# Kernel tuning notes

Measured on AMD Instinct MI355X. Metric: run time of the kernel, lower is better.

Reference implementation:

```python
import jax, jax.numpy as jnp
import numpy as np

# Problem constants (match init_kwargs)
A = 64          # particles
H = 1024        # hidden width
B = 512         # batch of configurations
V0 = -5.0
SIGMA0 = 0.5
GAUSS_CONST = V0 / (np.sqrt(2.0 * np.pi) * SIGMA0)
INV_2SIG2 = 1.0 / (2.0 * SIGMA0 * SIGMA0)


def setup_inputs() -> dict:
    key = jax.random.key(0)
    ks = jax.random.split(key, 7)
    x = jax.random.normal(ks[0], (B, A), dtype=jnp.float32)
    # 3-layer tanh MLP params: log|psi| = MLP(x) -> scalar
    W1 = jax.random.normal(ks[1], (A, H), dtype=jnp.float32) / np.sqrt(A)
    b1 = jnp.zeros((H,), dtype=jnp.float32)
    W2 = jax.random.normal(ks[2], (H, H), dtype=jnp.float32) / np.sqrt(H)
    b2 = jnp.zeros((H,), dtype=jnp.float32)
    W3 = jax.random.normal(ks[3], (H, 1), dtype=jnp.float32) / np.sqrt(H)
    b3 = jnp.zeros((1,), dtype=jnp.float32)
    return {"x": x, "W1": W1, "b1": b1, "W2": W2, "b2": b2, "W3": W3, "b3": b3}


def _logabs(W1, b1, W2, b2, W3, b3, xs):
    # xs: [A] -> scalar log|psi|
    h = jnp.tanh(xs @ W1 + b1)
    h = jnp.tanh(h @ W2 + b2)
    return (h @ W3 + b3)[0]


def reference(x, W1, b1, W2, b2, W3, b3):
    def logabs(xs):
        return _logabs(W1, b1, W2, b2, W3, b3, xs)

    grad_fn = jax.grad(logabs)  # reverse-mode, like jacrev

    def per_sample(xs):
        g = grad_fn(xs)                       # [A]   dlogabs/dx
        hess = jax.jacrev(grad_fn)(xs)        # [A,A] nested jacrev (backward-over-backward)
        lap = jnp.trace(hess) + jnp.sum(g * g)
        kin = -0.5 * lap
        pot = 0.5 * jnp.sum(xs * xs)
        d = xs[None, :] - xs[:, None]          # [A,A] pairwise differences
        gint = GAUSS_CONST * jnp.sum(jnp.triu(jnp.exp(-(d * d) * INV_2SIG2), k=1))
        return kin + pot + gint

    return jax.vmap(per_sample)(x)  # [B] local energies
```

## Files before the change

kernel.cpp:

```cpp
#include <hip/hip_runtime.h>
#include <hip/hip_bf16.h>
#include <stdint.h>

#define AN 64
#define HN 1024
#define BN 512
#define GAUSS_CONST (-3.989422804014327f)
#define INV_2SIG2 2.0f

#define SA 192.0f
#define SB 768.0f
#define INVQ (1.0f / (SA * SB))

typedef __attribute__((ext_vector_type(8))) short short8;
typedef __attribute__((ext_vector_type(4))) short short4v;
typedef __attribute__((ext_vector_type(4))) float floatx4;
typedef __attribute__((ext_vector_type(4))) int intx4;

__device__ inline unsigned short f2bf(float f) {
  __hip_bfloat16 h = __float2bfloat16(f);
  return *reinterpret_cast<unsigned short*>(&h);
}

__device__ inline unsigned q8(float x, float s) {
  float xc = fminf(fmaxf(x * s, -127.f), 127.f);
  int qi = (int)rintf(xc);
  return (unsigned)(qi & 255);
}

__device__ inline void gload_lds16(const void* g, void* l) {
  __builtin_amdgcn_global_load_lds(
      (const __attribute__((address_space(1))) void*)g,
      (__attribute__((address_space(3))) void*)l, 16, 0, 0);
}

#define PH_BAR  asm volatile("s_barrier" ::: "memory")
#define WAITV2  asm volatile("s_waitcnt vmcnt(2)" ::: "memory")
#define WAITV0  asm volatile("s_waitcnt vmcnt(0)" ::: "memory")

__global__ __launch_bounds__(256) void k1(
    const float* __restrict__ x, const float* __restrict__ W1,
    const float* __restrict__ b1, const float* __restrict__ W2,
    unsigned short* __restrict__ h1bf, float* __restrict__ t1f,
    float* __restrict__ a1, float* __restrict__ potgint,
    unsigned char* __restrict__ Pi8, unsigned short* __restrict__ W2T,
    unsigned short* __restrict__ W2bf, unsigned char* __restrict__ W2Ti8,
    float* __restrict__ W1T) {
  __shared__ float tile[64][65];
  __shared__ float xs[AN];
  __shared__ float red[4];
  int b = blockIdx.x, tid = threadIdx.x;
  if (b < BN) {
    int s = b;
    if (tid < AN) xs[tid] = x[s * AN + tid];
    __syncthreads();
    int j4 = tid * 4;
    floatx4 z4 = *reinterpret_cast<const floatx4*>(&b1[j4]);
    floatx4 cs4 = (floatx4){0.f, 0.f, 0.f, 0.f};
    for (int a = 0; a < AN; ++a) {
      floatx4 w = *reinterpret_cast<const floatx4*>(&W1[(size_t)a * HN + j4]);
      float xa = xs[a];
      #pragma unroll
      for (int e = 0; e < 4; ++e) { z4[e] += xa * w[e]; cs4[e] += w[e] * w[e]; }
    }
    floatx4 t4, a4; short4v h4;
    #pragma unroll
    for (int e = 0; e < 4; ++e) {
      float h = tanhf(z4[e]), t = 1.f - h * h;
      h4[e] = (short)f2bf(h);
      t4[e] = t;
      a4[e] = cs4[e] * h * t;
    }
    *reinterpret_cast<short4v*>(&h1bf[(size_t)s * HN + j4]) = h4;
    *reinterpret_cast<floatx4*>(&t1f[(size_t)s * HN + j4]) = t4;
    *reinterpret_cast<floatx4*>(&a1[(size_t)s * HN + j4]) = a4;
    float val = 0.f;
    #pragma unroll
    for (int p = 0; p < 16; ++p) {
      int idx = tid + p * 256;
      int i = idx >> 6, jj = idx & 63;
      if (jj > i) { float d = xs[i] - xs[jj]; val += __expf(-INV_2SIG2 * d * d); }
    }
    val *= GAUSS_CONST;
    if (tid < AN) val += 0.5f * xs[tid] * xs[tid];
    #pragma unroll
    for (int o = 32; o > 0; o >>= 1) val += __shfl_down(val, o, 64);
    if ((tid & 63) == 0) red[tid >> 6] = val;
    __syncthreads();
    if (tid == 0) potgint[s] = red[0] + red[1] + red[2] + red[3];
    size_t outBase = ((size_t)s * 64) * HN + j4;
    for (int a = 0; a < AN; ++a) {
      floatx4 w = *reinterpret_cast<const floatx4*>(&W1[(size_t)a * HN + j4]);
      unsigned p = q8(w[0] * t4[0], SA)
                 | (q8(w[1] * t4[1], SA) << 8)
                 | (q8(w[2] * t4[2], SA) << 16)
                 | (q8(w[3] * t4[3], SA) << 24);
      *reinterpret_cast<unsigned*>(&Pi8[outBase + (size_t)a * HN]) = p;
    }
  } else if (b < BN + 256) {
    int t = b - BN;
    int jt = (t >> 4) * 64, kt = (t & 15) * 64;
    #pragma unroll
    for (int it = 0; it < 4; ++it) {
      int e = it * 256 + tid;
      int r = e >> 4, cv = (e & 15) * 4;
      floatx4 v = *reinterpret_cast<const floatx4*>(&W2[(size_t)(jt + r) * HN + kt + cv]);
      tile[r][cv] = v[0]; tile[r][cv + 1] = v[1];
      tile[r][cv + 2] = v[2]; tile[r][cv + 3] = v[3];
      short4v o;
      #pragma unroll
      for (int i = 0; i < 4; ++i) o[i] = (short)f2bf(v[i]);
      *reinterpret_cast<short4v*>(&W2bf[(size_t)(jt + r) * HN + kt + cv]) = o;
    }
    __syncthreads();
    #pragma unroll
    for (int it = 0; it < 4; ++it) {
      int e = it * 256 + tid;
      int r = e >> 4, cv = (e & 15) * 4;
      float v0 = tile[cv][r], v1 = tile[cv + 1][r];
      float v2 = tile[cv + 2][r], v3 = tile[cv + 3][r];
      short4v o;
      o[0] = (short)f2bf(v0); o[1] = (short)f2bf(v1);
      o[2] = (short)f2bf(v2); o[3] = (short)f2bf(v3);
      *reinterpret_cast<short4v*>(&W2T[(size_t)(kt + r) * HN + jt + cv]) = o;
      unsigned p8 = q8(v0, SB) | (q8(v1, SB) << 8)
                  | (q8(v2, SB) << 16) | (q8(v3, SB) << 24);
      *reinterpret_cast<unsigned*>(&W2Ti8[(size_t)(kt + r) * HN + jt + cv]) = p8;
    }
  } else {
    int t = b - (BN + 256);
    int j0 = t * 64;
    #pragma unroll
    for (int it = 0; it < 4; ++it) {
      int e = it * 256 + tid;
      int r = e >> 4, cv = (e & 15) * 4;
      floatx4 v = *reinterpret_cast<const floatx4*>(&W1[(size_t)r * HN + j0 + cv]);
      tile[r][cv] = v[0]; tile[r][cv + 1] = v[1];
      tile[r][cv + 2] = v[2]; tile[r][cv + 3] = v[3];
    }
    __syncthreads();
    #pragma unroll
    for (int it = 0; it < 4; ++it) {
      int e = it * 256 + tid;
      int r = e >> 4, cv = (e & 15) * 4;
      floatx4 o;
      #pragma unroll
      for (int i = 0; i < 4; ++i) o[i] = tile[cv + i][r];
      *reinterpret_cast<floatx4*>(&W1T[(size_t)(j0 + r) * AN + cv]) = o;
    }
  }
}

__global__ __launch_bounds__(256) void k_z2(
    const unsigned short* __restrict__ h1bf, const unsigned short* __restrict__ W2T,
    const float* __restrict__ b2, const float* __restrict__ W3,
    float* __restrict__ dcoef, unsigned short* __restrict__ vbf) {
  __shared__ float redL[4 * 16 * 64];
  int n0 = blockIdx.x * 64, m0 = blockIdx.y * 16;
  int tid = threadIdx.x, w = tid >> 6, l = tid & 63, lr = l & 15, kg = l >> 4;
  floatx4 acc[4];
  #pragma unroll
  for (int nf = 0; nf < 4; ++nf) acc[nf] = (floatx4){0.f, 0.f, 0.f, 0.f};
  int arow = m0 + lr;
  for (int kt = 0; kt < 8; ++kt) {
    int kb = w * 256 + kt * 32 + kg * 8;
    short8 af = *reinterpret_cast<const short8*>(&h1bf[arow * HN + kb]);
    #pragma unroll
    for (int nf = 0; nf < 4; ++nf) {
      short8 bf_ = *reinterpret_cast<const short8*>(&W2T[(n0 + nf * 16 + lr) * HN + kb]);
      acc[nf] = __builtin_amdgcn_mfma_f32_16x16x32_bf16(af, bf_, acc[nf], 0, 0, 0);
    }
  }
  #pragma unroll
  for (int nf = 0; nf < 4; ++nf)
    #pragma unroll
    for (int r = 0; r < 4; ++r)
      redL[w * 1024 + (kg * 4 + r) * 64 + nf * 16 + lr] = acc[nf][r];
  __syncthreads();
  #pragma unroll
  for (int t = 0; t < 4; ++t) {
    int e = tid + t * 256;
    float z = redL[e] + redL[1024 + e] + redL[2048 + e] + redL[3072 + e];
    int row = e >> 6, col = e & 63;
    int s = m0 + row, k2 = n0 + col;
    z += b2[k2];
    float h = tanhf(z), tt = 1.f - h * h, w3 = W3[k2];
    dcoef[s * HN + k2] = -2.f * h * tt * w3;
    vbf[s * HN + k2] = f2bf(tt * w3);
  }
}

__global__ __launch_bounds__(512, 2) void k_bigw(
    const unsigned char* __restrict__ Pi8,
    const unsigned char* __restrict__ W2Ti8,
    float* __restrict__ q,
    const unsigned short* __restrict__ vbf, const unsigned short* __restrict__ W2bf,
    float* __restrict__ wbuf) {
  extern __shared__ unsigned char sm8[];
  int bid = blockIdx.x;
  int tid = threadIdx.x;

  if (bid < 512) {
    int xcd = bid & 7, local = bid >> 3;
    int px = local & 3;
    int py = xcd * 16 + (local >> 2);

    int wid = tid >> 6, l = tid & 63;
    int lr = l & 15, kg = l >> 4;
    int wr = wid >> 2, wc = wid & 3;
    int wr128 = wr * 128, wc64 = wc * 64;
    int rdOff = ((kg ^ ((lr >> 1) & 3)) << 4);

    int r1 = tid >> 2;
    int c1 = (tid & 3) ^ ((tid >> 3) & 3);
    const unsigned char* aSrc = &Pi8[(size_t)(py * 256 + r1) * HN + c1 * 16];
    const unsigned char* bSrc = &W2Ti8[(size_t)(px * 256 + r1) * HN + c1 * 16];

    auto stA = [&](int slot, int tt) {
      const unsigned char* s = aSrc + tt * 64;
      unsigned char* d = &sm8[slot * 16384 + tid * 16];
      gload_lds16(s, d);
      gload_lds16(s + (size_t)128 * HN, d + 8192);
    };
    auto stB = [&](int buf, int tt) {
      const unsigned char* s = bSrc + tt * 64;
      unsigned char* d = &sm8[49152 + buf * 16384 + tid * 16];
      gload_lds16(s, d);
      gload_lds16(s + (size_t)128 * HN, d + 8192);
    };

    intx4 acc[8][4];
    #pragma unroll
    for (int m = 0; m < 8; ++m)
      #pragma unroll
      for (int n = 0; n < 4; ++n) acc[m][n] = (intx4){0, 0, 0, 0};

    intx4 af[8], bfr[2];
    auto ldA = [&](int slot) {
      const unsigned char* Ap = &sm8[slot * 16384];
      #pragma unroll
      for (int m = 0; m < 8; ++m)
        af[m] = *reinterpret_cast<const intx4*>(&Ap[(wr128 + m * 16 + lr) * 64 + rdOff]);
    };
    auto ldB = [&](int buf, int nh) {
      const unsigned char* Bp = &sm8[49152 + buf * 16384];
      #pragma unroll
      for (int n = 0; n < 2; ++n)
        bfr[n] = *reinterpret_cast<const intx4*>(
            &Bp[(wc64 + (nh * 2 + n) * 16 + lr) * 64 + rdOff]);
    };
    auto mm = [&](int nh) {
      __builtin_amdgcn_s_setprio(1);
      #pragma unroll
      for (int m = 0; m < 8; ++m)
        #pragma unroll
        for (int n = 0; n < 2; ++n)
          acc[m][nh * 2 + n] = __builtin_amdgcn_mfma_i32_16x16x64_i8(
              af[m], bfr[n], acc[m][nh * 2 + n], 0, 0, 0);
      __builtin_amdgcn_s_setprio(0);
    };

    stA(0, 0); stB(0, 0); stA(1, 1);
    WAITV2; PH_BAR;

    int rs = 0;
    for (int t = 0; t < 16; ++t) {
      int rb = t & 1, wb = rb ^ 1;
      int ws = rs + 2; if (ws >= 3) ws -= 3;
      int tb = (t + 1 < 16) ? t + 1 : 15;
      int ta = (t + 2 < 16) ? t + 2 : 15;
      ldA(rs); ldB(rb, 0);
      stB(wb, tb);
      PH_BAR; mm(0); PH_BAR;
      ldB(rb, 1);
      stA(ws, ta);
      WAITV2;
      PH_BAR; mm(1); PH_BAR;
      rs = (rs + 1 == 3) ? 0 : rs + 1;
    }
    WAITV0;

    int colBase = px * 256 + wc64;
    #pragma unroll
    for (int half = 0; half < 2; ++half) {
      int sOut = py * 4 + wr * 2 + half;
      #pragma unroll
      for (int nf = 0; nf < 4; ++nf) {
        float v = 0.f;
        #pragma unroll
        for (int mf = half * 4; mf < half * 4 + 4; ++mf)
          #pragma unroll
          for (int r = 0; r < 4; ++r) {
            float mi = (float)acc[mf][nf][r] * INVQ;
            v += mi * mi;
          }
        v += __shfl_xor(v, 16, 64);
        v += __shfl_xor(v, 32, 64);
        if (l < 16) q[(size_t)sOut * HN + colBase + nf * 16 + l] = v;
      }
    }
  } else {
    float* redF = reinterpret_cast<float*>(sm8);
    int wi = bid - 512;
    int m0 = (wi >> 3) * 16, n0 = (wi & 7) * 128;
    int w = tid >> 6, l = tid & 63, lr = l & 15, kg = l >> 4;
    int ks = w >> 1, ch = w & 1;
    floatx4 acc[4];
    #pragma unroll
    for (int nf = 0; nf < 4; ++nf) acc[nf] = (floatx4){0.f, 0.f, 0.f, 0.f};
    int arow = m0 + lr;
    for (int kt = 0; kt < 8; ++kt) {
      int kb = ks * 256 + kt * 32 + kg * 8;
      short8 af = *reinterpret_cast<const short8*>(&vbf[arow * HN + kb]);
      #pragma unroll
      for (int nf = 0; nf < 4; ++nf) {
        short8 bf_ = *reinterpret_cast<const short8*>(
            &W2bf[(size_t)(n0 + ch * 64 + nf * 16 + lr) * HN + kb]);
        acc[nf] = __builtin_amdgcn_mfma_f32_16x16x32_bf16(af, bf_, acc[nf], 0, 0, 0);
      }
    }
    #pragma unroll
    for (int nf = 0; nf < 4; ++nf)
      #pragma unroll
      for (int r = 0; r < 4; ++r)
        redF[w * 1024 + (kg * 4 + r) * 64 + nf * 16 + lr] = acc[nf][r];
    __syncthreads();
    #pragma unroll
    for (int it = 0; it < 4; ++it) {
      int e = it * 512 + tid;
      int row = e >> 7, col = e & 127;
      int ch2 = col >> 6, cc = col & 63;
      float z = redF[(0 * 2 + ch2) * 1024 + row * 64 + cc]
              + redF[(1 * 2 + ch2) * 1024 + row * 64 + cc]
              + redF[(2 * 2 + ch2) * 1024 + row * 64 + cc]
              + redF[(3 * 2 + ch2) * 1024 + row * 64 + cc];
      wbuf[(size_t)(m0 + row) * HN + n0 + col] = z;
    }
  }
}

__global__ __launch_bounds__(256) void k_fin(
    const float* __restrict__ wbuf, const float* __restrict__ a1,
    const float* __restrict__ dcoef, const float* __restrict__ q,
    const float* __restrict__ t1f, const float* __restrict__ W1T,
    const float* __restrict__ potgint, float* __restrict__ out) {
  __shared__ float s_lds[HN];
  __shared__ float gl[256];
  __shared__ float red1[4], red2[4];
  int s = blockIdx.x, tid = threadIdx.x;
  float p1 = 0.f, p2 = 0.f;
  #pragma unroll
  for (int cc = 0; cc < 4; ++cc) {
    int j = tid + cc * 256;
    float wv = wbuf[s * HN + j];
    p1 += a1[s * HN + j] * wv;
    p2 += dcoef[s * HN + j] * q[s * HN + j];
    s_lds[j] = t1f[s * HN + j] * wv;
  }
  __syncthreads();
  int part = tid >> 6, a = tid & 63;
  float gp = 0.f;
  for (int jj = part * 256; jj < part * 256 + 256; ++jj)
    gp += s_lds[jj] * W1T[jj * AN + a];
  gl[tid] = gp;
  #pragma unroll
  for (int o = 32; o > 0; o >>= 1) { p1 += __shfl_down(p1, o, 64); p2 += __shfl_down(p2, o, 64); }
  if ((tid & 63) == 0) { red1[tid >> 6] = p1; red2[tid >> 6] = p2; }
  __syncthreads();
  if (tid < 64) {
    float g = gl[tid] + gl[64 + tid] + gl[128 + tid] + gl[192 + tid];
    float sq = g * g;
    #pragma unroll
    for (int o = 32; o > 0; o >>= 1) sq += __shfl_down(sq, o, 64);
    if (tid == 0) {
      float T1 = -2.f * (red1[0] + red1[1] + red1[2] + red1[3]);
      float T2 = red2[0] + red2[1] + red2[2] + red2[3];
      out[s] = -0.5f * (T1 + T2 + sq) + potgint[s];
    }
  }
}

extern "C" void kernel_launch(void* const* d_in, const int* in_sizes, int n_in,
                              void* d_out, int out_size, void* d_ws, size_t ws_size,
                              hipStream_t stream) {
  const float* x  = (const float*)d_in[0];
  const float* W1 = (const float*)d_in[1];
  const float* b1 = (const float*)d_in[2];
  const float* W2 = (const float*)d_in[3];
  const float* b2 = (const float*)d_in[4];
  const float* W3 = (const float*)d_in[5];
  float* out = (float*)d_out;

  char* ws = (char*)d_ws;
  size_t off = 0;
  auto alloc = [&](size_t bytes) -> void* {
    void* p = ws + off; off += (bytes + 255) & ~(size_t)255; return p;
  };
  unsigned short* W2T  = (unsigned short*)alloc((size_t)HN * HN * 2);
  unsigned short* W2bf = (unsigned short*)alloc((size_t)HN * HN * 2);
  unsigned char*  W2Ti8= (unsigned char*)alloc((size_t)HN * HN);
  float*          W1T  = (float*)alloc((size_t)AN * HN * 4);
  unsigned short* h1bf = (unsigned short*)alloc((size_t)BN * HN * 2);
  float*          t1f  = (float*)alloc((size_t)BN * HN * 4);
  float*          a1   = (float*)alloc((size_t)BN * HN * 4);
  float*          dcoef= (float*)alloc((size_t)BN * HN * 4);
  unsigned short* vbf  = (unsigned short*)alloc((size_t)BN * HN * 2);
  float*          wbuf = (float*)alloc((size_t)BN * HN * 4);
  float*          q    = (float*)alloc((size_t)BN * HN * 4);
  float*          pg   = (float*)alloc((size_t)BN * 4);
  unsigned char*  Pi8  = (unsigned char*)alloc((size_t)BN * AN * HN);

  static bool attrSet = false;
  if (!attrSet) {
    hipFuncSetAttribute((const void*)k_bigw,
                        hipFuncAttributeMaxDynamicSharedMemorySize, 81920);
    attrSet = true;
  }

  k1<<<dim3(BN + 256 + 16), 256, 0, stream>>>(x, W1, b1, W2,
                                              h1bf, t1f, a1, pg,
                                              Pi8, W2T, W2bf, W2Ti8, W1T);
  k_z2<<<dim3(HN / 64, BN / 16), 256, 0, stream>>>(h1bf, W2T, b2, W3, dcoef, vbf);
  k_bigw<<<dim3(512 + 256), 512, 81920, stream>>>(Pi8, W2Ti8, q, vbf, W2bf, wbuf);
  k_fin<<<dim3(BN), 256, 0, stream>>>(wbuf, a1, dcoef, q, t1f, W1T, pg, out);
}
```

Baseline: 173.2 us.

## Move Pi8 quantization from k1 into extra blocks of the z2 GEMM kernel

```diff
diff --git a/kernel.cpp b/kernel.cpp
--- a/kernel.cpp
+++ b/kernel.cpp
@@ -43,7 +43,7 @@
     const float* __restrict__ b1, const float* __restrict__ W2,
     unsigned short* __restrict__ h1bf, float* __restrict__ t1f,
     float* __restrict__ a1, float* __restrict__ potgint,
-    unsigned char* __restrict__ Pi8, unsigned short* __restrict__ W2T,
+    unsigned short* __restrict__ W2T,
     unsigned short* __restrict__ W2bf, unsigned char* __restrict__ W2Ti8,
     float* __restrict__ W1T) {
   __shared__ float tile[64][65];
@@ -57,6 +57,7 @@
     int j4 = tid * 4;
     floatx4 z4 = *reinterpret_cast<const floatx4*>(&b1[j4]);
     floatx4 cs4 = (floatx4){0.f, 0.f, 0.f, 0.f};
+    #pragma unroll 4
     for (int a = 0; a < AN; ++a) {
       floatx4 w = *reinterpret_cast<const floatx4*>(&W1[(size_t)a * HN + j4]);
       float xa = xs[a];
@@ -88,15 +89,6 @@
     if ((tid & 63) == 0) red[tid >> 6] = val;
     __syncthreads();
     if (tid == 0) potgint[s] = red[0] + red[1] + red[2] + red[3];
-    size_t outBase = ((size_t)s * 64) * HN + j4;
-    for (int a = 0; a < AN; ++a) {
-      floatx4 w = *reinterpret_cast<const floatx4*>(&W1[(size_t)a * HN + j4]);
-      unsigned p = q8(w[0] * t4[0], SA)
-                 | (q8(w[1] * t4[1], SA) << 8)
-                 | (q8(w[2] * t4[2], SA) << 16)
-                 | (q8(w[3] * t4[3], SA) << 24);
-      *reinterpret_cast<unsigned*>(&Pi8[outBase + (size_t)a * HN]) = p;
-    }
   } else if (b < BN + 256) {
     int t = b - BN;
     int jt = (t >> 4) * 64, kt = (t & 15) * 64;
@@ -151,42 +143,63 @@
   }
 }
 
-__global__ __launch_bounds__(256) void k_z2(
+__global__ __launch_bounds__(256) void k_z2p(
     const unsigned short* __restrict__ h1bf, const unsigned short* __restrict__ W2T,
     const float* __restrict__ b2, const float* __restrict__ W3,
-    float* __restrict__ dcoef, unsigned short* __restrict__ vbf) {
+    float* __restrict__ dcoef, unsigned short* __restrict__ vbf,
+    const float* __restrict__ W1, const float* __restrict__ t1f,
+    unsigned char* __restrict__ Pi8) {
   __shared__ float redL[4 * 16 * 64];
-  int n0 = blockIdx.x * 64, m0 = blockIdx.y * 16;
-  int tid = threadIdx.x, w = tid >> 6, l = tid & 63, lr = l & 15, kg = l >> 4;
-  floatx4 acc[4];
-  #pragma unroll
-  for (int nf = 0; nf < 4; ++nf) acc[nf] = (floatx4){0.f, 0.f, 0.f, 0.f};
-  int arow = m0 + lr;
-  for (int kt = 0; kt < 8; ++kt) {
-    int kb = w * 256 + kt * 32 + kg * 8;
-    short8 af = *reinterpret_cast<const short8*>(&h1bf[arow * HN + kb]);
-    #pragma unroll
-    for (int nf = 0; nf < 4; ++nf) {
-      short8 bf_ = *reinterpret_cast<const short8*>(&W2T[(n0 + nf * 16 + lr) * HN + kb]);
-      acc[nf] = __builtin_amdgcn_mfma_f32_16x16x32_bf16(af, bf_, acc[nf], 0, 0, 0);
-    }
-  }
-  #pragma unroll
-  for (int nf = 0; nf < 4; ++nf)
-    #pragma unroll
-    for (int r = 0; r < 4; ++r)
-      redL[w * 1024 + (kg * 4 + r) * 64 + nf * 16 + lr] = acc[nf][r];
-  __syncthreads();
-  #pragma unroll
-  for (int t = 0; t < 4; ++t) {
-    int e = tid + t * 256;
-    float z = redL[e] + redL[1024 + e] + redL[2048 + e] + redL[3072 + e];
-    int row = e >> 6, col = e & 63;
-    int s = m0 + row, k2 = n0 + col;
-    z += b2[k2];
-    float h = tanhf(z), tt = 1.f - h * h, w3 = W3[k2];
-    dcoef[s * HN + k2] = -2.f * h * tt * w3;
-    vbf[s * HN + k2] = f2bf(tt * w3);
+  int bid = blockIdx.x, tid = threadIdx.x;
+  if (bid < 512) {
+    int n0 = (bid & 15) * 64, m0 = (bid >> 4) * 16;
+    int w = tid >> 6, l = tid & 63, lr = l & 15, kg = l >> 4;
+    floatx4 acc[4];
+    #pragma unroll
+    for (int nf = 0; nf < 4; ++nf) acc[nf] = (floatx4){0.f, 0.f, 0.f, 0.f};
+    int arow = m0 + lr;
+    for (int kt = 0; kt < 8; ++kt) {
+      int kb = w * 256 + kt * 32 + kg * 8;
+      short8 af = *reinterpret_cast<const short8*>(&h1bf[arow * HN + kb]);
+      #pragma unroll
+      for (int nf = 0; nf < 4; ++nf) {
+        short8 bf_ = *reinterpret_cast<const short8*>(&W2T[(n0 + nf * 16 + lr) * HN + kb]);
+        acc[nf] = __builtin_amdgcn_mfma_f32_16x16x32_bf16(af, bf_, acc[nf], 0, 0, 0);
+      }
+    }
+    #pragma unroll
+    for (int nf = 0; nf < 4; ++nf)
+      #pragma unroll
+      for (int r = 0; r < 4; ++r)
+        redL[w * 1024 + (kg * 4 + r) * 64 + nf * 16 + lr] = acc[nf][r];
+    __syncthreads();
+    #pragma unroll
+    for (int t = 0; t < 4; ++t) {
+      int e = tid + t * 256;
+      float z = redL[e] + redL[1024 + e] + redL[2048 + e] + redL[3072 + e];
+      int row = e >> 6, col = e & 63;
+      int s = m0 + row, k2 = n0 + col;
+      z += b2[k2];
+      float h = tanhf(z), tt = 1.f - h * h, w3 = W3[k2];
+      dcoef[s * HN + k2] = -2.f * h * tt * w3;
+      vbf[s * HN + k2] = f2bf(tt * w3);
+    }
+  } else {
+    int p = bid - 512;
+    int s = p >> 1, a0 = (p & 1) * 32;
+    int j4 = tid * 4;
+    floatx4 t4 = *reinterpret_cast<const floatx4*>(&t1f[(size_t)s * HN + j4]);
+    size_t outBase = ((size_t)s * 64 + a0) * HN + j4;
+    #pragma unroll 8
+    for (int ai = 0; ai < 32; ++ai) {
+      int a = a0 + ai;
+      floatx4 w = *reinterpret_cast<const floatx4*>(&W1[(size_t)a * HN + j4]);
+      unsigned pk = q8(w[0] * t4[0], SA)
+                  | (q8(w[1] * t4[1], SA) << 8)
+                  | (q8(w[2] * t4[2], SA) << 16)
+                  | (q8(w[3] * t4[3], SA) << 24);
+      *reinterpret_cast<unsigned*>(&Pi8[outBase + (size_t)ai * HN]) = pk;
+    }
   }
 }
 
@@ -419,8 +432,9 @@
 
   k1<<<dim3(BN + 256 + 16), 256, 0, stream>>>(x, W1, b1, W2,
                                               h1bf, t1f, a1, pg,
-                                              Pi8, W2T, W2bf, W2Ti8, W1T);
-  k_z2<<<dim3(HN / 64, BN / 16), 256, 0, stream>>>(h1bf, W2T, b2, W3, dcoef, vbf);
+                                              W2T, W2bf, W2Ti8, W1T);
+  k_z2p<<<dim3(512 + 1024), 256, 0, stream>>>(h1bf, W2T, b2, W3, dcoef, vbf,
+                                              W1, t1f, Pi8);
   k_bigw<<<dim3(512 + 256), 512, 81920, stream>>>(Pi8, W2Ti8, q, vbf, W2bf, wbuf);
   k_fin<<<dim3(BN), 256, 0, stream>>>(wbuf, a1, dcoef, q, t1f, W1T, pg, out);
 }
```

New measurement: 145.9 us. 15.8% less time.
